# Optimization experiments

Hardware: AMD Instinct MI355X
Metric: run time of the kernel (lower is better)

Reference implementation:

```python
import jax, jax.numpy as jnp
import numpy as np

DIM = 1024
D_STATE = 16
D_CONV = 4
EXPAND = 2
D_INNER = EXPAND * DIM          # 2048
DT_RANK = DIM // 16             # 64 (ceil(1024/16))
BATCH = 4096
LN_EPS = 1e-5


def setup_inputs() -> dict:
    key = jax.random.key(0)
    ks = jax.random.split(key, 8)
    s = lambda k, shape, sc=0.02: (jax.random.normal(k, shape, jnp.float32) * sc)
    return {
        "x": jax.random.normal(ks[0], (BATCH, DIM), jnp.float32),
        "ln_gamma": jnp.ones((DIM,), jnp.float32),
        "ln_beta": jnp.zeros((DIM,), jnp.float32),
        "W_in": s(ks[1], (2 * D_INNER, DIM)),            # in_proj (no bias)
        "conv_w": s(ks[2], (D_INNER, D_CONV), 0.2),      # depthwise causal conv
        "conv_b": jnp.zeros((D_INNER,), jnp.float32),
        "W_xproj": s(ks[3], (DT_RANK + 2 * D_STATE, D_INNER)),
        "W_dt": s(ks[4], (D_INNER, DT_RANK), 0.1),
        "b_dt": s(ks[5], (D_INNER,), 0.5),
        "A_log": jnp.log(jnp.broadcast_to(
            jnp.arange(1, D_STATE + 1, dtype=jnp.float32), (D_INNER, D_STATE))),
        "Dskip": jnp.ones((D_INNER,), jnp.float32),
        "W_out": s(ks[6], (DIM, D_INNER)),               # out_proj (no bias)
    }


def _mamba_layer(x, ln_gamma, ln_beta, W_in, conv_w, conv_b,
                 W_xproj, W_dt, b_dt, A_log, Dskip, W_out):
    # x: [B, dim] -> unsqueeze(1): [B, L=1, dim]
    xs = x[:, None, :]
    # LayerNorm over last dim
    mu = jnp.mean(xs, axis=-1, keepdims=True)
    var = jnp.var(xs, axis=-1, keepdims=True)
    xn = (xs - mu) * jax.lax.rsqrt(var + LN_EPS) * ln_gamma + ln_beta
    # in_proj -> split into x, z   [B, L, d_inner] each
    xz = jnp.einsum('bld,ed->ble', xn, W_in)
    xi, z = jnp.split(xz, 2, axis=-1)
    L = xi.shape[1]
    # depthwise causal conv1d (kernel d_conv, left pad d_conv-1)
    xp = jnp.pad(xi, ((0, 0), (D_CONV - 1, 0), (0, 0)))
    xc = conv_b + sum(conv_w[:, k] * xp[:, k:k + L, :] for k in range(D_CONV))
    xc = jax.nn.silu(xc)
    # x_proj -> dt, B, C
    xdb = jnp.einsum('bld,ed->ble', xc, W_xproj)
    dt, Bm, Cm = jnp.split(xdb, [DT_RANK, DT_RANK + D_STATE], axis=-1)
    dt = jax.nn.softplus(jnp.einsum('blr,dr->bld', dt, W_dt) + b_dt)  # [B,L,d_inner]
    A = -jnp.exp(A_log)                                              # [d_inner,d_state]
    dA = jnp.exp(dt[..., None] * A)                                  # [B,L,d_inner,d_state]
    dBu = dt[..., None] * Bm[:, :, None, :] * xc[..., None]          # [B,L,d_inner,d_state]

    def step(h, inp):
        dA_l, dBu_l, C_l = inp
        h = dA_l * h + dBu_l                    # [B,d_inner,d_state]
        y = jnp.einsum('bdn,bn->bd', h, C_l)    # [B,d_inner]
        return h, y

    h0 = jnp.zeros((x.shape[0], D_INNER, D_STATE), x.dtype)
    _, ys = jax.lax.scan(step, h0, (dA.swapaxes(0, 1), dBu.swapaxes(0, 1), Cm.swapaxes(0, 1)))
    y = ys.swapaxes(0, 1) + Dskip * xc          # [B,L,d_inner]
    y = y * jax.nn.silu(z)
    out = jnp.einsum('ble,de->bld', y, W_out)   # [B,L,dim]
    return out[:, 0, :]                          # squeeze(1)


def reference(x, ln_gamma, ln_beta, W_in, conv_w, conv_b,
              W_xproj, W_dt, b_dt, A_log, Dskip, W_out):
    return _mamba_layer(x, ln_gamma, ln_beta, W_in, conv_w, conv_b,
                        W_xproj, W_dt, b_dt, A_log, Dskip, W_out)
```

## Files before the change

kernel.cpp:

```cpp
#include <hip/hip_runtime.h>
#include <hip/hip_bf16.h>
#include <stdint.h>

#define DIM     1024
#define DINNER  2048
#define BATCH   4096
#define LN_EPS  1e-5f

typedef unsigned short u16;
using f32x4  = __attribute__((ext_vector_type(4))) float;
using bf16x8 = __attribute__((ext_vector_type(8))) __bf16;

__device__ __forceinline__ float bf2f(u16 h) {
    union { unsigned u; float f; } v; v.u = ((unsigned)h) << 16; return v.f;
}
__device__ __forceinline__ u16 f2bf(float f) {
    union { float f; unsigned u; } v; v.f = f;
    unsigned r = v.u + 0x7fffu + ((v.u >> 16) & 1u);
    return (u16)(r >> 16);
}
__device__ __forceinline__ float silu_f(float x) {
    return x / (1.f + __expf(-x));
}

#define AS1 __attribute__((address_space(1)))
#define AS3 __attribute__((address_space(3)))

__device__ __forceinline__ unsigned lds_u32(const void* p) {
    return (unsigned)(unsigned long long)(const AS3 void*)p;
}

__global__ __launch_bounds__(256)
void cvt_ln(const float* __restrict__ x, const float* __restrict__ gamma,
            const float* __restrict__ beta, u16* __restrict__ xn,
            const float4* __restrict__ s0, ushort4* __restrict__ d0, int n0,
            const float4* __restrict__ s1, ushort4* __restrict__ d1, int n1,
            const float4* __restrict__ s2, ushort4* __restrict__ d2, int n2,
            const float4* __restrict__ s3, ushort4* __restrict__ d3, int n3)
{
    const int t = threadIdx.x;
    if (blockIdx.x < BATCH) {
        const int row = blockIdx.x;
        float4 v = ((const float4*)(x + (size_t)row * DIM))[t];
        float s1v = v.x + v.y + v.z + v.w;
        float s2v = v.x*v.x + v.y*v.y + v.z*v.z + v.w*v.w;
        #pragma unroll
        for (int o = 32; o > 0; o >>= 1) {
            s1v += __shfl_down(s1v, o);
            s2v += __shfl_down(s2v, o);
        }
        __shared__ float red[8];
        __shared__ float mv[2];
        const int w = t >> 6, l = t & 63;
        if (l == 0) { red[w] = s1v; red[4 + w] = s2v; }
        __syncthreads();
        if (t == 0) {
            float a = red[0] + red[1] + red[2] + red[3];
            float b = red[4] + red[5] + red[6] + red[7];
            float mu = a * (1.f / DIM);
            float var = b * (1.f / DIM) - mu * mu;
            mv[0] = mu; mv[1] = rsqrtf(var + LN_EPS);
        }
        __syncthreads();
        const float mu = mv[0], rs = mv[1];
        float4 g  = ((const float4*)gamma)[t];
        float4 be = ((const float4*)beta)[t];
        ushort4 o = make_ushort4(
            f2bf((v.x - mu) * rs * g.x + be.x),
            f2bf((v.y - mu) * rs * g.y + be.y),
            f2bf((v.z - mu) * rs * g.z + be.z),
            f2bf((v.w - mu) * rs * g.w + be.w));
        *(ushort4*)(xn + (size_t)row * DIM + t * 4) = o;
    } else {
        int i = (blockIdx.x - BATCH) * 256 + t;
        const int stride = (gridDim.x - BATCH) * 256;
        const int total = n0 + n1 + n2 + n3;
        for (; i < total; i += stride) {
            int j = i; const float4* s; ushort4* d;
            if (j < n0) { s = s0; d = d0; }
            else { j -= n0;
                if (j < n1) { s = s1; d = d1; }
                else { j -= n1;
                    if (j < n2) { s = s2; d = d2; }
                    else { j -= n2; s = s3; d = d3; }
                }
            }
            float4 v = s[j];
            d[j] = make_ushort4(f2bf(v.x), f2bf(v.y), f2bf(v.z), f2bf(v.w));
        }
    }
}

#define DSR(d, adr, OFFSTR) \
    asm volatile("ds_read_b128 %0, %1 offset:" OFFSTR : "=v"(d) : "v"(adr))
#define RD_A8(DST, A0, A1, S0, S1, S2, S3) do { \
    DSR(DST[0][0], A0, S0); DSR(DST[0][1], A1, S0); \
    DSR(DST[1][0], A0, S1); DSR(DST[1][1], A1, S1); \
    DSR(DST[2][0], A0, S2); DSR(DST[2][1], A1, S2); \
    DSR(DST[3][0], A0, S3); DSR(DST[3][1], A1, S3); } while (0)
#define RD_B4(DST, A0, A1, S0, S1) do { \
    DSR(DST[0][0], A0, S0); DSR(DST[0][1], A1, S0); \
    DSR(DST[1][0], A0, S1); DSR(DST[1][1], A1, S1); } while (0)

#define BC8(x) __builtin_bit_cast(bf16x8, x)
#define MF1(C, Av, Bv) C = __builtin_amdgcn_mfma_f32_16x16x32_bf16(BC8(Av), BC8(Bv), C, 0, 0, 0)

#define CL32_LO do { \
    _Pragma("unroll") for (int m = 0; m < 4; ++m) \
    _Pragma("unroll") for (int n = 0; n < 2; ++n) \
    _Pragma("unroll") for (int k = 0; k < 2; ++k) { \
        MF1(acc[m][n],     aLo[m][k], bC0[n][k]); \
        MF1(acc[m][n + 2], aLo[m][k], bC1[n][k]); } } while (0)
#define CL16_HI0 do { \
    _Pragma("unroll") for (int m = 0; m < 4; ++m) \
    _Pragma("unroll") for (int n = 0; n < 2; ++n) \
    _Pragma("unroll") for (int k = 0; k < 2; ++k) \
        MF1(acc[4 + m][n], aHi[m][k], bC0[n][k]); } while (0)
#define CL16_HI1 do { \
    _Pragma("unroll") for (int m = 0; m < 4; ++m) \
    _Pragma("unroll") for (int n = 0; n < 2; ++n) \
    _Pragma("unroll") for (int k = 0; k < 2; ++k) \
        MF1(acc[4 + m][n + 2], aHi[m][k], bC1[n][k]); } while (0)

#define WAIT_LGKM8 do { asm volatile("s_waitcnt lgkmcnt(8)" ::: "memory"); \
    __builtin_amdgcn_sched_barrier(0); } while (0)
#define WAIT_LGKM0 do { asm volatile("s_waitcnt lgkmcnt(0)" ::: "memory"); \
    __builtin_amdgcn_sched_barrier(0); } while (0)

#define TILE_BODY(CA0, CA1, NA0, NA1, NB0, NB1, SDA0, SDA1, SDB0, SDB1, KT) do { \
    RD_A8(aHi, CA0, CA1, "8192", "10240", "12288", "14336"); \
    WAIT_LGKM8; \
    __builtin_amdgcn_s_setprio(1); CL32_LO; __builtin_amdgcn_s_setprio(0); \
    WAIT_LGKM0; \
    asm volatile("s_waitcnt vmcnt(0)" ::: "memory"); \
    __builtin_amdgcn_s_barrier(); \
    stage(SDB0, Bb, KT); stage(SDB1, BbH, KT); \
    stage(SDA0, Ab, KT); stage(SDA1, AbH, KT); \
    __builtin_amdgcn_s_setprio(1); CL16_HI0; __builtin_amdgcn_s_setprio(0); \
    RD_B4(bC0, NB0, NB1, "0", "2048"); \
    RD_A8(aLo, NA0, NA1, "0", "2048", "4096", "6144"); \
    __builtin_amdgcn_s_setprio(1); CL16_HI1; __builtin_amdgcn_s_setprio(0); \
    RD_B4(bC1, NB0, NB1, "4096", "6144"); \
} while (0)

__global__ __launch_bounds__(512, 2)
void gemmP(const u16* __restrict__ A, const u16* __restrict__ B,
           int N, int K, int nkt,
           u16* __restrict__ dst0, u16* __restrict__ dst1,
           const float* __restrict__ conv_w, const float* __restrict__ conv_b)
{
    __shared__ __align__(16) u16 lds[2][4][8192];
    const int tid = threadIdx.x;
    const int wid = tid >> 6, l = tid & 63;
    const int wm = wid >> 2, wn = wid & 3;
    const int lr = l & 15, l16 = l >> 4;
    const int brow = blockIdx.y * 256, bcol = blockIdx.x * 256;

    const int sr = tid >> 3;
    const int skk = ((tid & 7) ^ (sr & 7)) * 8;
    const u16* Ab  = A + (size_t)(brow + sr) * K + skk;
    const u16* Bb  = B + (size_t)(bcol + sr) * K + skk;
    const u16* AbH = Ab + (size_t)128 * K;
    const u16* BbH = Bb + (size_t)128 * K;

    u16* const dA0h0 = &lds[0][0][tid * 8]; u16* const dA0h1 = &lds[0][1][tid * 8];
    u16* const dA1h0 = &lds[1][0][tid * 8]; u16* const dA1h1 = &lds[1][1][tid * 8];
    u16* const dB0h0 = &lds[0][2][tid * 8]; u16* const dB0h1 = &lds[0][3][tid * 8];
    u16* const dB1h0 = &lds[1][2][tid * 8]; u16* const dB1h1 = &lds[1][3][tid * 8];

    const unsigned cxb0 = (unsigned)(((0 + l16) ^ (l & 7)) * 16);
    const unsigned cxb1 = (unsigned)(((4 + l16) ^ (l & 7)) * 16);
    const unsigned aB0 = lds_u32(&lds[0][wm][0]) + (unsigned)(lr * 128);
    const unsigned bB0 = lds_u32(&lds[0][2 + (wn >> 1)][0]) + (unsigned)((wn & 1) * 8192 + lr * 128);
    const unsigned adA00 = aB0 + cxb0, adA01 = aB0 + cxb1;
    const unsigned adA10 = adA00 + 65536, adA11 = adA01 + 65536;
    const unsigned adB00 = bB0 + cxb0, adB01 = bB0 + cxb1;
    const unsigned adB10 = adB00 + 65536, adB11 = adB01 + 65536;

    f32x4 acc[8][4] = {};
    float4 aLo[4][2], aHi[4][2], bC0[2][2], bC1[2][2];

    auto stage = [&](u16* dst, const u16* srcrow, int kt) {
        const u16* s = srcrow + (size_t)kt * 64;
        __builtin_amdgcn_global_load_lds((const AS1 void*)s, (AS3 void*)dst, 16, 0, 0);
        __builtin_amdgcn_global_load_lds((const AS1 void*)(s + (size_t)64 * K),
                                         (AS3 void*)(dst + 4096), 16, 0, 0);
    };

    stage(dB0h0, Bb, 0);  stage(dB0h1, BbH, 0);
    stage(dA0h0, Ab, 0);  stage(dA0h1, AbH, 0);
    stage(dB1h0, Bb, 1);  stage(dB1h1, BbH, 1);
    stage(dA1h0, Ab, 1);  stage(dA1h1, AbH, 1);
    asm volatile("s_waitcnt vmcnt(8)" ::: "memory");
    __builtin_amdgcn_s_barrier();
    RD_B4(bC0, adB00, adB01, "0", "2048");
    RD_B4(bC1, adB00, adB01, "4096", "6144");
    RD_A8(aLo, adA00, adA01, "0", "2048", "4096", "6144");

    const int niter = nkt >> 1;
    for (int i = 0; i < niter; ++i) {
        const int T = 2 * i;
        const int k2 = (T + 2 < nkt) ? T + 2 : nkt - 1;
        const int k3 = (T + 3 < nkt) ? T + 3 : nkt - 1;
        TILE_BODY(adA00, adA01, adA10, adA11, adB10, adB11,
                  dA0h0, dA0h1, dB0h0, dB0h1, k2);
        TILE_BODY(adA10, adA11, adA00, adA01, adB00, adB01,
                  dA1h0, dA1h1, dB1h0, dB1h1, k3);
    }

    asm volatile("s_waitcnt vmcnt(0) lgkmcnt(0)" ::: "memory");
    __builtin_amdgcn_s_barrier();

    float cb[4], cw[4];
    const bool isxc = (bcol < DINNER);
    if (isxc) {
        #pragma unroll
        for (int n = 0; n < 4; ++n) {
            const int cg = bcol + wn * 64 + n * 16 + lr;
            cb[n] = conv_b[cg]; cw[n] = conv_w[cg * 4 + 3];
        }
    }
    u16* eb = &lds[0][0][0];
    #pragma unroll
    for (int m = 0; m < 8; ++m)
        #pragma unroll
        for (int n = 0; n < 4; ++n)
            #pragma unroll
            for (int r = 0; r < 4; ++r) {
                const int rl = wm * 128 + m * 16 + l16 * 4 + r;
                const int cl = wn * 64 + n * 16 + lr;
                float v = acc[m][n][r];
                v = isxc ? silu_f(cb[n] + cw[n] * v) : silu_f(v);
                eb[rl * 256 + cl] = f2bf(v);
            }
    __syncthreads();

    u16* base = isxc ? (dst0 + bcol) : (dst1 + (bcol - DINNER));
    #pragma unroll
    for (int it = 0; it < 16; ++it) {
        const int idx = it * 4096 + tid * 8;
        const int r = idx >> 8, c = idx & 255;
        *(uint4*)(base + (size_t)(brow + r) * DINNER + c) = *(const uint4*)(eb + idx);
    }
}

__global__ __launch_bounds__(256)
void gemm_xproj(const u16* __restrict__ xcb, const u16* __restrict__ Wx,
                float* __restrict__ P)
{
    __shared__ __align__(16) u16 Xs[64 * 64];
    __shared__ __align__(16) u16 Ws[96 * 64];
    const int t = threadIdx.x, w = t >> 6, l = t & 63;
    const int brow = blockIdx.x * 64;
    const int ks = blockIdx.y;
    const int lr = l & 15, l16 = l >> 4;
    const int skk = ((l & 7) ^ (l >> 3)) * 8;
    const u16* Xbase = xcb + (size_t)(brow + (l >> 3)) * DINNER + skk;
    const u16* Wbase = Wx + (size_t)(l >> 3) * DINNER + skk;

    f32x4 acc[6] = {};
    const int kend = ks * 512 + 512;
    for (int k0 = ks * 512; k0 < kend; k0 += 64) {
        #pragma unroll
        for (int c = 0; c < 2; ++c) {
            const int seg = c * 4 + w;
            __builtin_amdgcn_global_load_lds(
                (const AS1 void*)(Xbase + (size_t)seg * 8 * DINNER + k0),
                (AS3 void*)(&Xs[seg * 512]), 16, 0, 0);
        }
        #pragma unroll
        for (int c = 0; c < 3; ++c) {
            const int seg = c * 4 + w;
            __builtin_amdgcn_global_load_lds(
                (const AS1 void*)(Wbase + (size_t)seg * 8 * DINNER + k0),
                (AS3 void*)(&Ws[seg * 512]), 16, 0, 0);
        }
        __syncthreads();
        #pragma unroll
        for (int kk = 0; kk < 2; ++kk) {
            const int ra = w * 16 + lr;
            bf16x8 av = *(const bf16x8*)(&Xs[ra * 64 + (((kk * 4 + l16) ^ (ra & 7)) * 8)]);
            #pragma unroll
            for (int n = 0; n < 6; ++n) {
                const int rb = n * 16 + lr;
                bf16x8 bv = *(const bf16x8*)(&Ws[rb * 64 + (((kk * 4 + l16) ^ (rb & 7)) * 8)]);
                acc[n] = __builtin_amdgcn_mfma_f32_16x16x32_bf16(av, bv, acc[n], 0, 0, 0);
            }
        }
        __syncthreads();
    }
    #pragma unroll
    for (int n = 0; n < 6; ++n)
        #pragma unroll
        for (int r = 0; r < 4; ++r) {
            const int row = brow + w * 16 + l16 * 4 + r;
            const int col = n * 16 + lr;
            P[((size_t)ks * 96 + col) * BATCH + row] = acc[n][r];
        }
}

__global__ __launch_bounds__(256)
void finish_xdb(const float* __restrict__ P, u16* __restrict__ dtb, float* __restrict__ sbuf)
{
    const int b = blockIdx.x * 256 + threadIdx.x;
    #pragma unroll 8
    for (int c = 0; c < 64; ++c) {
        float v = P[((size_t)0 * 96 + c) * BATCH + b] + P[((size_t)1 * 96 + c) * BATCH + b]
                + P[((size_t)2 * 96 + c) * BATCH + b] + P[((size_t)3 * 96 + c) * BATCH + b];
        dtb[(size_t)b * 64 + c] = f2bf(v);
    }
    float s = 0.f;
    for (int n = 0; n < 16; ++n) {
        float Bv = 0.f, Cv = 0.f;
        #pragma unroll
        for (int ks = 0; ks < 4; ++ks) {
            Bv += P[((size_t)ks * 96 + 64 + n) * BATCH + b];
            Cv += P[((size_t)ks * 96 + 80 + n) * BATCH + b];
        }
        s += Bv * Cv;
    }
    sbuf[b] = s;
}

__global__ __launch_bounds__(256)
void gemm_dt_y(const u16* __restrict__ dtb, const u16* __restrict__ Wdt,
               const float* __restrict__ b_dt, const float* __restrict__ Dskip,
               const float* __restrict__ s,
               const u16* __restrict__ xcb, const u16* __restrict__ szb,
               u16* __restrict__ y)
{
    __shared__ __align__(16) u16 Ds[64 * 64];
    __shared__ __align__(16) u16 Ws[128 * 64];
    const int t = threadIdx.x, w = t >> 6, l = t & 63;
    const int wr = w >> 1, wc = w & 1;
    const int brow = blockIdx.y * 64;
    const int bcol = blockIdx.x * 128;
    const int lr = l & 15, l16 = l >> 4;
    const int skk = ((l & 7) ^ (l >> 3)) * 8;

    {
        const u16* Dbase = dtb + (size_t)(brow + (l >> 3)) * 64 + skk;
        const u16* Wbase = Wdt + (size_t)(bcol + (l >> 3)) * 64 + skk;
        #pragma unroll
        for (int c = 0; c < 2; ++c) {
            const int seg = c * 4 + w;
            __builtin_amdgcn_global_load_lds(
                (const AS1 void*)(Dbase + (size_t)seg * 8 * 64),
                (AS3 void*)(&Ds[seg * 512]), 16, 0, 0);
        }
        #pragma unroll
        for (int c = 0; c < 4; ++c) {
            const int seg = c * 4 + w;
            __builtin_amdgcn_global_load_lds(
                (const AS1 void*)(Wbase + (size_t)seg * 8 * 64),
                (AS3 void*)(&Ws[seg * 512]), 16, 0, 0);
        }
    }
    __syncthreads();

    f32x4 acc[2][4] = {};
    #pragma unroll
    for (int kk = 0; kk < 2; ++kk) {
        bf16x8 av[2], bv[4];
        #pragma unroll
        for (int m = 0; m < 2; ++m) {
            const int r = wr * 32 + m * 16 + lr;
            av[m] = *(const bf16x8*)(&Ds[r * 64 + (((kk * 4 + l16) ^ (r & 7)) * 8)]);
        }
        #pragma unroll
        for (int n = 0; n < 4; ++n) {
            const int r = wc * 64 + n * 16 + lr;
            bv[n] = *(const bf16x8*)(&Ws[r * 64 + (((kk * 4 + l16) ^ (r & 7)) * 8)]);
        }
        #pragma unroll
        for (int m = 0; m < 2; ++m)
            #pragma unroll
            for (int n = 0; n < 4; ++n)
                acc[m][n] = __builtin_amdgcn_mfma_f32_16x16x32_bf16(av[m], bv[n], acc[m][n], 0, 0, 0);
    }

    #pragma unroll
    for (int m = 0; m < 2; ++m)
        #pragma unroll
        for (int n = 0; n < 4; ++n)
            #pragma unroll
            for (int r = 0; r < 4; ++r) {
                const int row = brow + wr * 32 + m * 16 + l16 * 4 + r;
                const int col = bcol + wc * 64 + n * 16 + lr;
                float v = acc[m][n][r] + b_dt[col];
                float dt = (v > 20.f) ? v : log1pf(__expf(v));
                float xcv = bf2f(xcb[(size_t)row * DINNER + col]);
                float szv = bf2f(szb[(size_t)row * DINNER + col]);
                float yv = (dt * s[row] + Dskip[col]) * xcv * szv;
                y[(size_t)row * DINNER + col] = f2bf(yv);
            }
}

__global__ __launch_bounds__(256, 2)
void gemm4n(const u16* __restrict__ A, const u16* __restrict__ Bm,
            float* __restrict__ out)
{
    __shared__ __align__(16) u16 lds[2][12288];
    const int t = threadIdx.x, w = t >> 6, l = t & 63;
    const int wr = w >> 1, wc = w & 1;
    const int lr = l & 15, l16 = l >> 4;
    const int brow = blockIdx.y * 64, bcol = blockIdx.x * 128;
    const int K = DINNER, nkt = 32;

    auto stage = [&](int buf, int kt) {
        #pragma unroll
        for (int c = 0; c < 2; ++c) {
            const int o = c * 256 + t;
            const int sr = o >> 3;
            const int sc = (o & 7) ^ (sr & 7);
            __builtin_amdgcn_global_load_lds(
                (const AS1 void*)(A + (size_t)(brow + sr) * K + kt * 64 + sc * 8),
                (AS3 void*)(&lds[buf][o * 8]), 16, 0, 0);
        }
        #pragma unroll
        for (int c = 0; c < 4; ++c) {
            const int o = c * 256 + t;
            const int sr = o >> 3;
            const int sc = (o & 7) ^ (sr & 7);
            __builtin_amdgcn_global_load_lds(
                (const AS1 void*)(Bm + (size_t)(bcol + sr) * K + kt * 64 + sc * 8),
                (AS3 void*)(&lds[buf][4096 + o * 8]), 16, 0, 0);
        }
    };

    f32x4 acc[2][4] = {};

    stage(0, 0);
    stage(1, 1);
    asm volatile("s_waitcnt vmcnt(6)" ::: "memory");
    __builtin_amdgcn_s_barrier();

    for (int kt = 0; kt < nkt; ++kt) {
        const int cur = kt & 1;
        #pragma unroll
        for (int kk = 0; kk < 2; ++kk) {
            bf16x8 af[2], bf[4];
            #pragma unroll
            for (int m = 0; m < 2; ++m) {
                const int r = wr * 32 + m * 16 + lr;
                af[m] = *(const bf16x8*)(&lds[cur][r * 64 + (((kk * 4 + l16) ^ (r & 7)) * 8)]);
            }
            #pragma unroll
            for (int n = 0; n < 4; ++n) {
                const int r = wc * 64 + n * 16 + lr;
                bf[n] = *(const bf16x8*)(&lds[cur][4096 + r * 64 + (((kk * 4 + l16) ^ (r & 7)) * 8)]);
            }
            #pragma unroll
            for (int m = 0; m < 2; ++m)
                #pragma unroll
                for (int n = 0; n < 4; ++n)
                    acc[m][n] = __builtin_amdgcn_mfma_f32_16x16x32_bf16(af[m], bf[n], acc[m][n], 0, 0, 0);
        }
        __builtin_amdgcn_sched_barrier(0);
        __builtin_amdgcn_s_barrier();
        const int t2 = (kt + 2 < nkt) ? kt + 2 : nkt - 1;
        stage(cur, t2);
        asm volatile("s_waitcnt vmcnt(6)" ::: "memory");
        __builtin_amdgcn_sched_barrier(0);
        __builtin_amdgcn_s_barrier();
    }

    asm volatile("s_waitcnt vmcnt(0) lgkmcnt(0)" ::: "memory");
    __builtin_amdgcn_s_barrier();

    float* eb = (float*)&lds[0][0];
    #pragma unroll
    for (int m = 0; m < 2; ++m)
        #pragma unroll
        for (int n = 0; n < 4; ++n)
            #pragma unroll
            for (int r = 0; r < 4; ++r) {
                const int row = wr * 32 + m * 16 + l16 * 4 + r;
                const int col = wc * 64 + n * 16 + lr;
                eb[row * 128 + col] = acc[m][n][r];
            }
    __syncthreads();
    #pragma unroll
    for (int it = 0; it < 8; ++it) {
        const int idx = it * 1024 + t * 4;
        const int row = idx >> 7, col = idx & 127;
        *(float4*)(out + (size_t)(brow + row) * DIM + bcol + col) = *(const float4*)(eb + idx);
    }
}

extern "C" void kernel_launch(void* const* d_in, const int* in_sizes, int n_in,
                              void* d_out, int out_size, void* d_ws, size_t ws_size,
                              hipStream_t stream) {
    const float* x      = (const float*)d_in[0];
    const float* ln_g   = (const float*)d_in[1];
    const float* ln_b   = (const float*)d_in[2];
    const float* W_in   = (const float*)d_in[3];
    const float* conv_w = (const float*)d_in[4];
    const float* conv_b = (const float*)d_in[5];
    const float* W_xp   = (const float*)d_in[6];
    const float* W_dt   = (const float*)d_in[7];
    const float* b_dt   = (const float*)d_in[8];
    const float* Dskip  = (const float*)d_in[10];
    const float* W_out  = (const float*)d_in[11];
    float* out = (float*)d_out;

    char* ws = (char*)d_ws;
    const size_t MB = 1u << 20;
    u16*  W_in_b  = (u16*)(ws);
    u16*  xn      = (u16*)(ws + 8 * MB);
    u16*  xcb     = (u16*)(ws + 16 * MB);
    u16*  szb     = (u16*)(ws + 32 * MB);
    float* Pxp    = (float*)(ws + 48 * MB);
    u16*  W_xp_b  = (u16*)(ws + 55 * MB);
    u16*  W_dt_b  = (u16*)(ws + 56 * MB);
    u16*  dtb     = (u16*)(ws + 57 * MB);
    float* sbuf   = (float*)(ws + 58 * MB);
    u16*  W_out_b = (u16*)(ws + 64 * MB);
    u16*  yb      = (u16*)(ws + 68 * MB);

    cvt_ln<<<BATCH + 2048, 256, 0, stream>>>(
        x, ln_g, ln_b, xn,
        (const float4*)W_in,  (ushort4*)W_in_b,  (2 * DINNER * DIM) / 4,
        (const float4*)W_out, (ushort4*)W_out_b, (DIM * DINNER) / 4,
        (const float4*)W_xp,  (ushort4*)W_xp_b,  (96 * DINNER) / 4,
        (const float4*)W_dt,  (ushort4*)W_dt_b,  (DINNER * 64) / 4);

    gemmP<<<dim3(4096 / 256, BATCH / 256, 1), 512, 0, stream>>>(
        xn, W_in_b, 4096, DIM, DIM / 64, xcb, szb, conv_w, conv_b);

    gemm_xproj<<<dim3(BATCH / 64, 4), 256, 0, stream>>>(xcb, W_xp_b, Pxp);

    finish_xdb<<<BATCH / 256, 256, 0, stream>>>(Pxp, dtb, sbuf);

    gemm_dt_y<<<dim3(DINNER / 128, BATCH / 64), 256, 0, stream>>>(
        dtb, W_dt_b, b_dt, Dskip, sbuf, xcb, szb, yb);

    gemm4n<<<dim3(DIM / 128, BATCH / 64), 256, 0, stream>>>(yb, W_out_b, out);
}
```

Before: 145.3 us.

## Remap blocks per XCD, swizzle epilogue LDS, vectorize dt/y epilogue

Two GEMMs (gemmP and gemm4n) remap their linear block index so that blocks on the same XCD work on nearby tiles, which is meant to improve L2 reuse of A and B. Their epilogue LDS staging buffers get XOR swizzles to cut bank conflicts on the scatter writes. gemm_dt_y now stores softplus(dt) into a swizzled LDS tile and then does 16-byte vectorized loads of xc and z and stores of y, replacing scalar strided bf16 accesses. The remap hard-codes the grid shapes (16 and 8 blocks wide) and assumes the hardware assigns blocks to 8 XCDs round-robin.

Measured after the change: 146.0 us. Within noise of the previous version (+0.5%).

```diff
diff --git a/kernel.cpp b/kernel.cpp
--- a/kernel.cpp
+++ b/kernel.cpp
@@ -154,7 +154,12 @@
     const int wid = tid >> 6, l = tid & 63;
     const int wm = wid >> 2, wn = wid & 3;
     const int lr = l & 15, l16 = l >> 4;
-    const int brow = blockIdx.y * 256, bcol = blockIdx.x * 256;
+
+    const int lin = blockIdx.y * 16 + blockIdx.x;
+    const int xcd = lin & 7, q = lin >> 3;
+    const int by = (xcd & 3) * 4 + (q >> 3);
+    const int bx = (xcd >> 2) * 8 + (q & 7);
+    const int brow = by * 256, bcol = bx * 256;
 
     const int sr = tid >> 3;
     const int skk = ((tid & 7) ^ (sr & 7)) * 8;
@@ -231,7 +236,7 @@
                 const int cl = wn * 64 + n * 16 + lr;
                 float v = acc[m][n][r];
                 v = isxc ? silu_f(cb[n] + cw[n] * v) : silu_f(v);
-                eb[rl * 256 + cl] = f2bf(v);
+                eb[rl * 256 + (cl ^ ((rl & 15) << 4))] = f2bf(v);
             }
     __syncthreads();
 
@@ -240,7 +245,8 @@
     for (int it = 0; it < 16; ++it) {
         const int idx = it * 4096 + tid * 8;
         const int r = idx >> 8, c = idx & 255;
-        *(uint4*)(base + (size_t)(brow + r) * DINNER + c) = *(const uint4*)(eb + idx);
+        uint4 v = *(const uint4*)(eb + r * 256 + ((c ^ ((r & 15) << 4))));
+        *(uint4*)(base + (size_t)(brow + r) * DINNER + c) = v;
     }
 }
 
@@ -331,6 +337,7 @@
 {
     __shared__ __align__(16) u16 Ds[64 * 64];
     __shared__ __align__(16) u16 Ws[128 * 64];
+    __shared__ __align__(16) u16 dts[64 * 128];
     const int t = threadIdx.x, w = t >> 6, l = t & 63;
     const int wr = w >> 1, wc = w & 1;
     const int brow = blockIdx.y * 64;
@@ -385,15 +392,42 @@
         for (int n = 0; n < 4; ++n)
             #pragma unroll
             for (int r = 0; r < 4; ++r) {
-                const int row = brow + wr * 32 + m * 16 + l16 * 4 + r;
-                const int col = bcol + wc * 64 + n * 16 + lr;
-                float v = acc[m][n][r] + b_dt[col];
+                const int row = wr * 32 + m * 16 + l16 * 4 + r;
+                const int col = wc * 64 + n * 16 + lr;
+                float v = acc[m][n][r] + b_dt[bcol + col];
                 float dt = (v > 20.f) ? v : log1pf(__expf(v));
-                float xcv = bf2f(xcb[(size_t)row * DINNER + col]);
-                float szv = bf2f(szb[(size_t)row * DINNER + col]);
-                float yv = (dt * s[row] + Dskip[col]) * xcv * szv;
-                y[(size_t)row * DINNER + col] = f2bf(yv);
-            }
+                dts[row * 128 + (col ^ ((row & 7) << 4))] = f2bf(dt);
+            }
+    __syncthreads();
+
+    const int rlo = t >> 4;
+    const int cg  = (t & 15) * 8;
+    #pragma unroll
+    for (int rr = 0; rr < 4; ++rr) {
+        const int row = rr * 16 + rlo;
+        const int grow = brow + row;
+        const float sr = s[grow];
+        uint4 dv = *(const uint4*)(&dts[row * 128 + ((cg ^ ((row & 7) << 4)))]);
+        uint4 xv = *(const uint4*)(xcb + (size_t)grow * DINNER + bcol + cg);
+        uint4 zv = *(const uint4*)(szb + (size_t)grow * DINNER + bcol + cg);
+        float4 D0 = *(const float4*)(Dskip + bcol + cg);
+        float4 D1 = *(const float4*)(Dskip + bcol + cg + 4);
+        const float* Dp = &D0.x;
+        uint4 ov;
+        unsigned* op = (unsigned*)&ov;
+        #pragma unroll
+        for (int k = 0; k < 4; ++k) {
+            unsigned du = ((const unsigned*)&dv)[k];
+            unsigned xu = ((const unsigned*)&xv)[k];
+            unsigned zu = ((const unsigned*)&zv)[k];
+            float Da = (k < 2) ? Dp[2 * k]     : (&D1.x)[2 * (k - 2)];
+            float Db = (k < 2) ? Dp[2 * k + 1] : (&D1.x)[2 * (k - 2) + 1];
+            float y0 = (bf2f((u16)du) * sr + Da) * bf2f((u16)xu) * bf2f((u16)zu);
+            float y1 = (bf2f((u16)(du >> 16)) * sr + Db) * bf2f((u16)(xu >> 16)) * bf2f((u16)(zu >> 16));
+            op[k] = (unsigned)f2bf(y0) | ((unsigned)f2bf(y1) << 16);
+        }
+        *(uint4*)(y + (size_t)grow * DINNER + bcol + cg) = ov;
+    }
 }
 
 __global__ __launch_bounds__(256, 2)
@@ -404,7 +438,12 @@
     const int t = threadIdx.x, w = t >> 6, l = t & 63;
     const int wr = w >> 1, wc = w & 1;
     const int lr = l & 15, l16 = l >> 4;
-    const int brow = blockIdx.y * 64, bcol = blockIdx.x * 128;
+
+    const int lin = blockIdx.y * 8 + blockIdx.x;
+    const int xcd = lin & 7, q = lin >> 3;
+    const int by = xcd * 8 + (q >> 3);
+    const int bx = q & 7;
+    const int brow = by * 64, bcol = bx * 128;
     const int K = DINNER, nkt = 32;
 
     auto stage = [&](int buf, int kt) {
@@ -477,14 +516,15 @@
             for (int r = 0; r < 4; ++r) {
                 const int row = wr * 32 + m * 16 + l16 * 4 + r;
                 const int col = wc * 64 + n * 16 + lr;
-                eb[row * 128 + col] = acc[m][n][r];
+                eb[row * 128 + (col ^ ((row & 7) << 2))] = acc[m][n][r];
             }
     __syncthreads();
     #pragma unroll
     for (int it = 0; it < 8; ++it) {
         const int idx = it * 1024 + t * 4;
         const int row = idx >> 7, col = idx & 127;
-        *(float4*)(out + (size_t)(brow + row) * DIM + bcol + col) = *(const float4*)(eb + idx);
+        float4 v = *(const float4*)(eb + row * 128 + ((col ^ ((row & 7) << 2))));
+        *(float4*)(out + (size_t)(brow + row) * DIM + bcol + col) = v;
     }
 }
 
```
